# Performance work log

Hardware: AMD Instinct MI355X
Metric: run time of the kernel (lower is better)

The kernel has to match this reference:

```python
import jax, jax.numpy as jnp
import numpy as np

T, G, K, N = 8192, 8, 1024, 2048

def setup_inputs() -> dict:
    key = jax.random.key(0)
    k1, k2, k3 = jax.random.split(key, 3)
    x = jax.random.normal(k1, (T, K), dtype=jnp.float32)
    w = jax.random.normal(k2, (G, N, K), dtype=jnp.float32) * 0.02
    # cumulative end-offsets per group: sorted, last entry == T (covers all tokens)
    offs = jnp.sort(jax.random.randint(k3, (G,), 0, T).astype(jnp.int32))
    offs = offs.at[-1].set(T)
    return {"input": x, "weight": w, "grouped_mm_offs": offs}

def reference(input, weight, grouped_mm_offs):
    # grouped_mm(input, weight.transpose(1,2), offs): token t in group g iff
    # offs[g-1] <= t < offs[g]; out[t] = input[t] @ weight[g].T
    t = input.shape[0]
    g = weight.shape[0]
    gid = jnp.searchsorted(grouped_mm_offs, jnp.arange(t), side="right")  # [T]
    out = jnp.zeros((t, weight.shape[1]), dtype=input.dtype)
    for gi in range(g):  # fixed small expert loop; data dims stay vectorized
        xg = jnp.where((gid == gi)[:, None], input, jnp.zeros((), input.dtype))
        out = out + xg @ weight[gi].T
    return out
```

## Files before the change

### kernel.cpp

```cpp
#include <hip/hip_runtime.h>
#include <hip/hip_bf16.h>


#define T_DIM 8192
#define G_DIM 8
#define K_DIM 1024
#define N_DIM 2048

using short8 = __attribute__((ext_vector_type(8))) short;
using f32x4  = __attribute__((ext_vector_type(4))) float;

typedef __attribute__((address_space(1))) void gvoid;
typedef __attribute__((address_space(3))) void lvoid;

__global__ __launch_bounds__(256) void cvt_kernel(const float* __restrict__ src,
                                                  ushort4* __restrict__ dst,
                                                  int n4) {
  int i = blockIdx.x * blockDim.x + threadIdx.x;
  if (i >= n4) return;
  float4 v = reinterpret_cast<const float4*>(src)[i];
  ushort4 o;
  o.x = __builtin_bit_cast(unsigned short, __float2bfloat16(v.x));
  o.y = __builtin_bit_cast(unsigned short, __float2bfloat16(v.y));
  o.z = __builtin_bit_cast(unsigned short, __float2bfloat16(v.z));
  o.w = __builtin_bit_cast(unsigned short, __float2bfloat16(v.w));
  dst[i] = o;
}

template <bool MASKED>
__device__ __forceinline__ void tile_accum(const __hip_bfloat16* __restrict__ xb,
                                           const __hip_bfloat16* __restrict__ wg,
                                           __hip_bfloat16* As, __hip_bfloat16* Bs,
                                           f32x4 (&acc)[4][4],
                                           int m0, int n0, int lo, int hi) {
  const int lane = threadIdx.x & 63;
  const int wid  = threadIdx.x >> 6;
  const int wm   = wid >> 1;
  const int wn   = wid & 1;

  bool valid[4];
  if (MASKED) {
#pragma unroll
    for (int mt = 0; mt < 4; ++mt) {
      const int row = m0 + wm * 64 + mt * 16 + (lane & 15);
      valid[mt] = (row >= lo) && (row < hi);
    }
  }

  const int srow = lane >> 3;
  const int scol = (lane & 7) * 8;

  for (int kk = 0; kk < K_DIM / 64; ++kk) {
    const int k0 = kk * 64;
#pragma unroll
    for (int i = 0; i < 4; ++i) {
      const int j   = wid * 4 + i;
      const int row = j * 8 + srow;
      const __hip_bfloat16* ga = xb + (size_t)(m0 + row) * K_DIM + k0 + scol;
      const __hip_bfloat16* gb = wg + (size_t)(n0 + row) * K_DIM + k0 + scol;
      __builtin_amdgcn_global_load_lds((gvoid*)ga, (lvoid*)(As + j * 512), 16, 0, 0);
      __builtin_amdgcn_global_load_lds((gvoid*)gb, (lvoid*)(Bs + j * 512), 16, 0, 0);
    }
    __syncthreads();

#pragma unroll
    for (int ks = 0; ks < 64; ks += 32) {
      const int ko = ks + (lane >> 4) * 8;
      short8 a[4], b[4];
      short8 z = {};
#pragma unroll
      for (int mt = 0; mt < 4; ++mt) {
        a[mt] = *reinterpret_cast<const short8*>(
            As + (wm * 64 + mt * 16 + (lane & 15)) * 64 + ko);
        if (MASKED) {
          if (!valid[mt]) a[mt] = z;
        }
      }
#pragma unroll
      for (int nt = 0; nt < 4; ++nt) {
        b[nt] = *reinterpret_cast<const short8*>(
            Bs + (wn * 64 + nt * 16 + (lane & 15)) * 64 + ko);
      }
#pragma unroll
      for (int mt = 0; mt < 4; ++mt)
#pragma unroll
        for (int nt = 0; nt < 4; ++nt)
          acc[mt][nt] = __builtin_amdgcn_mfma_f32_16x16x32_bf16(
              a[mt], b[nt], acc[mt][nt], 0, 0, 0);
    }
    __syncthreads();
  }
}

__global__ __launch_bounds__(256) void grouped_gemm_kernel(
    const __hip_bfloat16* __restrict__ xb,
    const __hip_bfloat16* __restrict__ wb,
    const int* __restrict__ offs,
    float* __restrict__ out) {
  __shared__ __hip_bfloat16 As[128 * 64];
  __shared__ __hip_bfloat16 Bs[128 * 64];

  const int m0 = blockIdx.y * 128;
  const int n0 = blockIdx.x * 128;

  int offv[G_DIM];
#pragma unroll
  for (int g = 0; g < G_DIM; ++g) offv[g] = offs[g];

  int g_lo = 0;
  while (g_lo < G_DIM - 1 && offv[g_lo] <= m0) ++g_lo;
  int g_hi = g_lo;
  while (g_hi < G_DIM - 1 && offv[g_hi] <= m0 + 127) ++g_hi;

  f32x4 acc[4][4] = {};

  if (g_lo == g_hi) {
    tile_accum<false>(xb, wb + (size_t)g_lo * N_DIM * K_DIM, As, Bs, acc,
                      m0, n0, 0, 0);
  } else {
    for (int g = g_lo; g <= g_hi; ++g) {
      const int lo = g ? offv[g - 1] : 0;
      const int hi = offv[g];
      if (hi <= lo) continue;
      tile_accum<true>(xb, wb + (size_t)g * N_DIM * K_DIM, As, Bs, acc,
                       m0, n0, lo, hi);
    }
  }

  const int lane = threadIdx.x & 63;
  const int wid  = threadIdx.x >> 6;
  const int wm   = wid >> 1;
  const int wn   = wid & 1;
  const int quad = lane >> 4;
#pragma unroll
  for (int mt = 0; mt < 4; ++mt) {
#pragma unroll
    for (int nt = 0; nt < 4; ++nt) {
      const int row = m0 + wm * 64 + mt * 16 + quad * 4;
      const int col = n0 + wn * 64 + nt * 16 + (lane & 15);
#pragma unroll
      for (int r = 0; r < 4; ++r)
        out[(size_t)(row + r) * N_DIM + col] = acc[mt][nt][r];
    }
  }
}

__global__ __launch_bounds__(256) void fallback_kernel(
    const float* __restrict__ x, const float* __restrict__ w,
    const int* __restrict__ offs, float* __restrict__ out) {
  __shared__ float xs[K_DIM];
  const int t = blockIdx.y;
  int g = 0;
  while (g < G_DIM - 1 && offs[g] <= t) ++g;
  for (int i = threadIdx.x; i < K_DIM; i += blockDim.x)
    xs[i] = x[(size_t)t * K_DIM + i];
  __syncthreads();
  const int n = blockIdx.x * blockDim.x + threadIdx.x;
  const float* wr = w + ((size_t)g * N_DIM + n) * K_DIM;
  float s = 0.f;
  for (int k = 0; k < K_DIM; ++k) s += xs[k] * wr[k];
  out[(size_t)t * N_DIM + n] = s;
}

extern "C" void kernel_launch(void* const* d_in, const int* in_sizes, int n_in,
                              void* d_out, int out_size, void* d_ws, size_t ws_size,
                              hipStream_t stream) {
  const float* x    = (const float*)d_in[0];
  const float* w    = (const float*)d_in[1];
  const int*   offs = (const int*)d_in[2];
  float*       out  = (float*)d_out;

  const size_t x_elems = (size_t)T_DIM * K_DIM;
  const size_t w_elems = (size_t)G_DIM * N_DIM * K_DIM;
  const size_t need    = (x_elems + w_elems) * sizeof(__hip_bfloat16);

  if (ws_size < need) {
    fallback_kernel<<<dim3(N_DIM / 256, T_DIM), 256, 0, stream>>>(x, w, offs, out);
    return;
  }

  __hip_bfloat16* xb = (__hip_bfloat16*)d_ws;
  __hip_bfloat16* wb = xb + x_elems;

  const int n4x = (int)(x_elems / 4);
  const int n4w = (int)(w_elems / 4);
  cvt_kernel<<<n4x / 256, 256, 0, stream>>>(x, (ushort4*)xb, n4x);
  cvt_kernel<<<n4w / 256, 256, 0, stream>>>(w, (ushort4*)wb, n4w);

  grouped_gemm_kernel<<<dim3(N_DIM / 128, T_DIM / 128), 256, 0, stream>>>(
      xb, wb, offs, out);
}
```

Before: 216.1 us.

## Split grouped GEMM per group in grid z, swizzle LDS, merge conversion kernels

Adds a group index to the launch grid so each block computes one (group, tile) pair and exits early when the tile holds none of that group's rows. Boundary rows are masked at store time instead of zeroing A fragments. The LDS layout is XOR-swizzled to cut bank conflicts on fragment reads, and the two fp32-to-bf16 conversion launches are merged into one kernel that writes 8 elements per thread. The cost is many empty blocks that launch and immediately return. Boundary tiles are now handled by separate blocks that write disjoint rows, so no accumulation across blocks is needed.

```diff
diff --git a/kernel.cpp b/kernel.cpp
--- a/kernel.cpp
+++ b/kernel.cpp
@@ -7,48 +7,62 @@
 #define K_DIM 1024
 #define N_DIM 2048
 
-using short8 = __attribute__((ext_vector_type(8))) short;
-using f32x4  = __attribute__((ext_vector_type(4))) float;
+using short8  = __attribute__((ext_vector_type(8))) short;
+using f32x4   = __attribute__((ext_vector_type(4))) float;
+using ushort8 = __attribute__((ext_vector_type(8))) unsigned short;
 
 typedef __attribute__((address_space(1))) void gvoid;
 typedef __attribute__((address_space(3))) void lvoid;
 
-__global__ __launch_bounds__(256) void cvt_kernel(const float* __restrict__ src,
-                                                  ushort4* __restrict__ dst,
-                                                  int n4) {
+__global__ __launch_bounds__(256) void cvt_kernel(const float* __restrict__ x,
+                                                  const float* __restrict__ w,
+                                                  ushort8* __restrict__ xb,
+                                                  ushort8* __restrict__ wb,
+                                                  int n8x, int n8tot) {
   int i = blockIdx.x * blockDim.x + threadIdx.x;
-  if (i >= n4) return;
-  float4 v = reinterpret_cast<const float4*>(src)[i];
-  ushort4 o;
-  o.x = __builtin_bit_cast(unsigned short, __float2bfloat16(v.x));
-  o.y = __builtin_bit_cast(unsigned short, __float2bfloat16(v.y));
-  o.z = __builtin_bit_cast(unsigned short, __float2bfloat16(v.z));
-  o.w = __builtin_bit_cast(unsigned short, __float2bfloat16(v.w));
-  dst[i] = o;
+  if (i >= n8tot) return;
+  const float4* s; ushort8* d; int j;
+  if (i < n8x) { s = (const float4*)x; d = xb; j = i; }
+  else         { s = (const float4*)w; d = wb; j = i - n8x; }
+  float4 v0 = s[2 * j], v1 = s[2 * j + 1];
+  ushort8 o;
+  o[0] = __builtin_bit_cast(unsigned short, __float2bfloat16(v0.x));
+  o[1] = __builtin_bit_cast(unsigned short, __float2bfloat16(v0.y));
+  o[2] = __builtin_bit_cast(unsigned short, __float2bfloat16(v0.z));
+  o[3] = __builtin_bit_cast(unsigned short, __float2bfloat16(v0.w));
+  o[4] = __builtin_bit_cast(unsigned short, __float2bfloat16(v1.x));
+  o[5] = __builtin_bit_cast(unsigned short, __float2bfloat16(v1.y));
+  o[6] = __builtin_bit_cast(unsigned short, __float2bfloat16(v1.z));
+  o[7] = __builtin_bit_cast(unsigned short, __float2bfloat16(v1.w));
+  d[j] = o;
 }
 
-template <bool MASKED>
-__device__ __forceinline__ void tile_accum(const __hip_bfloat16* __restrict__ xb,
-                                           const __hip_bfloat16* __restrict__ wg,
-                                           __hip_bfloat16* As, __hip_bfloat16* Bs,
-                                           f32x4 (&acc)[4][4],
-                                           int m0, int n0, int lo, int hi) {
+__global__ __launch_bounds__(256) void grouped_gemm_kernel(
+    const __hip_bfloat16* __restrict__ xb,
+    const __hip_bfloat16* __restrict__ wb,
+    const int* __restrict__ offs,
+    float* __restrict__ out) {
+  const int g  = blockIdx.z;
+  const int m0 = blockIdx.y * 128;
+  const int n0 = blockIdx.x * 128;
+  const int lo = g ? offs[g - 1] : 0;
+  const int hi = offs[g];
+  if (lo >= m0 + 128 || hi <= m0 || hi <= lo) return;
+
+  __shared__ __align__(16) __hip_bfloat16 As[128 * 64];
+  __shared__ __align__(16) __hip_bfloat16 Bs[128 * 64];
+
+  const __hip_bfloat16* wg = wb + (size_t)g * N_DIM * K_DIM;
+
   const int lane = threadIdx.x & 63;
   const int wid  = threadIdx.x >> 6;
   const int wm   = wid >> 1;
   const int wn   = wid & 1;
 
-  bool valid[4];
-  if (MASKED) {
-#pragma unroll
-    for (int mt = 0; mt < 4; ++mt) {
-      const int row = m0 + wm * 64 + mt * 16 + (lane & 15);
-      valid[mt] = (row >= lo) && (row < hi);
-    }
-  }
+  const int srow = lane >> 3;
+  const int scol = ((lane & 7) ^ srow) * 8;
 
-  const int srow = lane >> 3;
-  const int scol = (lane & 7) * 8;
+  f32x4 acc[4][4] = {};
 
   for (int kk = 0; kk < K_DIM / 64; ++kk) {
     const int k0 = kk * 64;
@@ -64,23 +78,18 @@
     __syncthreads();
 
 #pragma unroll
-    for (int ks = 0; ks < 64; ks += 32) {
-      const int ko = ks + (lane >> 4) * 8;
+    for (int ks = 0; ks < 2; ++ks) {
+      const int kb  = ks * 4 + (lane >> 4);
+      const int off = ((kb ^ (lane & 7)) * 8);
       short8 a[4], b[4];
-      short8 z = {};
 #pragma unroll
-      for (int mt = 0; mt < 4; ++mt) {
+      for (int mt = 0; mt < 4; ++mt)
         a[mt] = *reinterpret_cast<const short8*>(
-            As + (wm * 64 + mt * 16 + (lane & 15)) * 64 + ko);
-        if (MASKED) {
-          if (!valid[mt]) a[mt] = z;
-        }
-      }
+            As + (wm * 64 + mt * 16 + (lane & 15)) * 64 + off);
 #pragma unroll
-      for (int nt = 0; nt < 4; ++nt) {
+      for (int nt = 0; nt < 4; ++nt)
         b[nt] = *reinterpret_cast<const short8*>(
-            Bs + (wn * 64 + nt * 16 + (lane & 15)) * 64 + ko);
-      }
+            Bs + (wn * 64 + nt * 16 + (lane & 15)) * 64 + off);
 #pragma unroll
       for (int mt = 0; mt < 4; ++mt)
 #pragma unroll
@@ -90,57 +99,20 @@
     }
     __syncthreads();
   }
-}
 
-__global__ __launch_bounds__(256) void grouped_gemm_kernel(
-    const __hip_bfloat16* __restrict__ xb,
-    const __hip_bfloat16* __restrict__ wb,
-    const int* __restrict__ offs,
-    float* __restrict__ out) {
-  __shared__ __hip_bfloat16 As[128 * 64];
-  __shared__ __hip_bfloat16 Bs[128 * 64];
-
-  const int m0 = blockIdx.y * 128;
-  const int n0 = blockIdx.x * 128;
-
-  int offv[G_DIM];
-#pragma unroll
-  for (int g = 0; g < G_DIM; ++g) offv[g] = offs[g];
-
-  int g_lo = 0;
-  while (g_lo < G_DIM - 1 && offv[g_lo] <= m0) ++g_lo;
-  int g_hi = g_lo;
-  while (g_hi < G_DIM - 1 && offv[g_hi] <= m0 + 127) ++g_hi;
-
-  f32x4 acc[4][4] = {};
-
-  if (g_lo == g_hi) {
-    tile_accum<false>(xb, wb + (size_t)g_lo * N_DIM * K_DIM, As, Bs, acc,
-                      m0, n0, 0, 0);
-  } else {
-    for (int g = g_lo; g <= g_hi; ++g) {
-      const int lo = g ? offv[g - 1] : 0;
-      const int hi = offv[g];
-      if (hi <= lo) continue;
-      tile_accum<true>(xb, wb + (size_t)g * N_DIM * K_DIM, As, Bs, acc,
-                       m0, n0, lo, hi);
-    }
-  }
-
-  const int lane = threadIdx.x & 63;
-  const int wid  = threadIdx.x >> 6;
-  const int wm   = wid >> 1;
-  const int wn   = wid & 1;
   const int quad = lane >> 4;
 #pragma unroll
   for (int mt = 0; mt < 4; ++mt) {
+    const int rbase = m0 + wm * 64 + mt * 16 + quad * 4;
 #pragma unroll
-    for (int nt = 0; nt < 4; ++nt) {
-      const int row = m0 + wm * 64 + mt * 16 + quad * 4;
-      const int col = n0 + wn * 64 + nt * 16 + (lane & 15);
+    for (int r = 0; r < 4; ++r) {
+      const int row = rbase + r;
+      if (row < lo || row >= hi) continue;
 #pragma unroll
-      for (int r = 0; r < 4; ++r)
-        out[(size_t)(row + r) * N_DIM + col] = acc[mt][nt][r];
+      for (int nt = 0; nt < 4; ++nt) {
+        const int col = n0 + wn * 64 + nt * 16 + (lane & 15);
+        out[(size_t)row * N_DIM + col] = acc[mt][nt][r];
+      }
     }
   }
 }
@@ -182,11 +154,11 @@
   __hip_bfloat16* xb = (__hip_bfloat16*)d_ws;
   __hip_bfloat16* wb = xb + x_elems;
 
-  const int n4x = (int)(x_elems / 4);
-  const int n4w = (int)(w_elems / 4);
-  cvt_kernel<<<n4x / 256, 256, 0, stream>>>(x, (ushort4*)xb, n4x);
-  cvt_kernel<<<n4w / 256, 256, 0, stream>>>(w, (ushort4*)wb, n4w);
+  const int n8x   = (int)(x_elems / 8);
+  const int n8tot = (int)((x_elems + w_elems) / 8);
+  cvt_kernel<<<(n8tot + 255) / 256, 256, 0, stream>>>(
+      x, w, (ushort8*)xb, (ushort8*)wb, n8x, n8tot);
 
-  grouped_gemm_kernel<<<dim3(N_DIM / 128, T_DIM / 128), 256, 0, stream>>>(
+  grouped_gemm_kernel<<<dim3(N_DIM / 128, T_DIM / 128, G_DIM), 256, 0, stream>>>(
       xb, wb, offs, out);
 }
```

After: 191.3 us. 11.5% less time.
